# Kernel tuning notes

Measured on AMD Instinct MI355X. Metric: run time of the kernel, lower is better.

The kernel has to match this reference:

```python
import jax, jax.numpy as jnp
import numpy as np

N_NODES = 50000
N_EDGES = 600000
IN_DIM = 128
OUT_DIM = 128
EPS = 1e-12  # guards sqrt grad at exactly-zero diffs (matches torch.norm subgradient behavior)


def setup_inputs() -> dict:
    key = jax.random.key(0)
    k1, k2, k3, k4, k5 = jax.random.split(key, 5)
    h = jax.random.normal(k1, (N_NODES, IN_DIM), dtype=jnp.float32)
    # xavier-uniform-ish scale for fc weight [out_dim, in_dim]
    lim = float(np.sqrt(6.0 / (IN_DIM + OUT_DIM)))
    W_fc = jax.random.uniform(k2, (OUT_DIM, IN_DIM), dtype=jnp.float32, minval=-lim, maxval=lim)
    beta = jax.random.uniform(k3, (1,), dtype=jnp.float32)  # Tensor(1).uniform_(0,1)
    src = jax.random.randint(k4, (N_EDGES,), 0, N_NODES, dtype=jnp.int32)
    dst = jax.random.randint(k5, (N_EDGES,), 0, N_NODES, dtype=jnp.int32)
    return {"h": h, "W_fc": W_fc, "beta": beta, "src": src, "dst": dst}


def reference(h, W_fc, beta, src, dst):
    n = h.shape[0]
    # z = fc(h)  (dropout omitted for determinism; see notes)
    z = h @ W_fc.T  # [N, out_dim]
    zs = z[src]     # [E, out_dim] gather
    zd = z[dst]     # [E, out_dim] gather
    # RBF edge attention: e = -beta * ||z_src - z_dst||_2
    sq = jnp.sum((zs - zd) ** 2, axis=1)          # [E]
    e = -beta[0] * jnp.sqrt(sq + EPS)             # [E]
    # segment softmax over incoming edges of each dst node
    m = jax.ops.segment_max(e, dst, num_segments=n)   # [N], -inf for empty
    ex = jnp.exp(e - m[dst])                          # [E]
    denom = jax.ops.segment_sum(ex, dst, num_segments=n)  # [N]
    alpha = ex / denom[dst]                           # [E]
    # scatter-weighted sum of src features into dst nodes
    h_out = jax.ops.segment_sum(alpha[:, None] * zs, dst, num_segments=n)  # [N, out_dim]
    return h_out
```

## Files before the change

kernel.cpp:

```cpp
#include <hip/hip_runtime.h>
#include <math.h>

#define N_NODES 50000
#define N_EDGES 600000
#define DIM 128
#define BCAP 64

typedef __attribute__((ext_vector_type(8))) short bf16x8;
typedef __attribute__((ext_vector_type(4))) float f32x4;

static __device__ __forceinline__ short f2bf(float f) {
    unsigned u = __float_as_uint(f);
    unsigned r = (u + 0x7FFFu + ((u >> 16) & 1u)) >> 16;
    return (short)r;
}

#define UNPK(w, d0, d1)                         \
    d0 = __uint_as_float((w) << 16);            \
    d1 = __uint_as_float((w) & 0xFFFF0000u);

__global__ __launch_bounds__(256) void prep_kernel(const float* __restrict__ W,
                                                   unsigned short* __restrict__ Wb,
                                                   int* __restrict__ cur,
                                                   int* __restrict__ cnt) {
    int gid = blockIdx.x * 256 + threadIdx.x;
    if (gid < N_NODES) {
        cur[gid] = 0;
        cnt[gid] = 0;
    }
    if (gid < DIM * DIM) Wb[gid] = (unsigned short)f2bf(W[gid]);
}

__global__ __launch_bounds__(256) void bfill_kernel(const int* __restrict__ src,
                                                    const int* __restrict__ dst,
                                                    int* __restrict__ cur,
                                                    int* __restrict__ lst) {
    int i = blockIdx.x * 256 + threadIdx.x;
    if (i >= N_EDGES) return;
    int d = dst[i];
    int pos = atomicAdd(cur + d, 1);
    if (pos < BCAP) lst[d * BCAP + pos] = src[i];
}

__global__ __launch_bounds__(256) void count_kernel(const int* __restrict__ dst,
                                                    int* __restrict__ cnt) {
    int i = blockIdx.x * 256 + threadIdx.x;
    if (i < N_EDGES) atomicAdd(cnt + dst[i], 1);
}

__global__ __launch_bounds__(256) void scan_a(const int* __restrict__ cnt,
                                              int* __restrict__ incl,
                                              int* __restrict__ bsum) {
    __shared__ int s[256];
    int i = blockIdx.x * 256 + threadIdx.x;
    s[threadIdx.x] = (i < N_NODES) ? cnt[i] : 0;
    __syncthreads();
    #pragma unroll
    for (int off = 1; off < 256; off <<= 1) {
        int t = (threadIdx.x >= off) ? s[threadIdx.x - off] : 0;
        __syncthreads();
        s[threadIdx.x] += t;
        __syncthreads();
    }
    if (i < N_NODES) incl[i] = s[threadIdx.x];
    if (threadIdx.x == 255) bsum[blockIdx.x] = s[255];
}

__global__ __launch_bounds__(256) void scan_b(int* __restrict__ bsum, int nb) {
    __shared__ int s[256];
    s[threadIdx.x] = (threadIdx.x < nb) ? bsum[threadIdx.x] : 0;
    __syncthreads();
    #pragma unroll
    for (int off = 1; off < 256; off <<= 1) {
        int t = (threadIdx.x >= off) ? s[threadIdx.x - off] : 0;
        __syncthreads();
        s[threadIdx.x] += t;
        __syncthreads();
    }
    if (threadIdx.x < nb) bsum[threadIdx.x] = s[threadIdx.x];
}

__global__ __launch_bounds__(256) void scan_c(int* __restrict__ incl_off,
                                              const int* __restrict__ cnt,
                                              const int* __restrict__ bsum) {
    int i = blockIdx.x * 256 + threadIdx.x;
    if (i >= N_NODES) return;
    int base = (blockIdx.x > 0) ? bsum[blockIdx.x - 1] : 0;
    incl_off[i] = incl_off[i] - cnt[i] + base;
}

__global__ __launch_bounds__(256) void cfill_kernel(const int* __restrict__ src,
                                                    const int* __restrict__ dst,
                                                    const int* __restrict__ off,
                                                    int* __restrict__ cur,
                                                    int* __restrict__ lst) {
    int i = blockIdx.x * 256 + threadIdx.x;
    if (i >= N_EDGES) return;
    int d = dst[i];
    int pos = atomicAdd(cur + d, 1);
    lst[off[d] + pos] = src[i];
}

__global__ __launch_bounds__(256) void gemm_kernel(const float* __restrict__ h,
                                                   const unsigned short* __restrict__ Wb,
                                                   unsigned short* __restrict__ zb) {
    int wave = blockIdx.x * 4 + (threadIdx.x >> 6);
    if (wave >= N_NODES / 16) return;
    int lane = threadIdx.x & 63;
    int lo = lane & 15;
    int hi = lane >> 4;
    long row0 = (long)wave * 16;

    bf16x8 afrag[4];
    const float* arow = h + (row0 + lo) * DIM;
    #pragma unroll
    for (int kt = 0; kt < 4; ++kt) {
        const float* ap = arow + kt * 32 + hi * 8;
        float4 f0 = *(const float4*)ap;
        float4 f1 = *(const float4*)(ap + 4);
        bf16x8 a;
        a[0] = f2bf(f0.x); a[1] = f2bf(f0.y); a[2] = f2bf(f0.z); a[3] = f2bf(f0.w);
        a[4] = f2bf(f1.x); a[5] = f2bf(f1.y); a[6] = f2bf(f1.z); a[7] = f2bf(f1.w);
        afrag[kt] = a;
    }

    #pragma unroll
    for (int ct = 0; ct < 8; ++ct) {
        f32x4 acc = {0.f, 0.f, 0.f, 0.f};
        const unsigned short* brow = Wb + (ct * 16 + lo) * DIM + hi * 8;
        #pragma unroll
        for (int kt = 0; kt < 4; ++kt) {
            bf16x8 b = *(const bf16x8*)(brow + kt * 32);
            acc = __builtin_amdgcn_mfma_f32_16x16x32_bf16(afrag[kt], b, acc, 0, 0, 0);
        }
        unsigned short* zp = zb + (row0 + hi * 4) * DIM + ct * 16 + lo;
        zp[0 * DIM] = (unsigned short)f2bf(acc[0]);
        zp[1 * DIM] = (unsigned short)f2bf(acc[1]);
        zp[2 * DIM] = (unsigned short)f2bf(acc[2]);
        zp[3 * DIM] = (unsigned short)f2bf(acc[3]);
    }
}

__global__ __launch_bounds__(256) void node_kernel(const unsigned short* __restrict__ zb,
                                                   const int* __restrict__ lst,
                                                   const int* __restrict__ off,
                                                   const int* __restrict__ degp,
                                                   int stride,
                                                   const float* __restrict__ beta,
                                                   float* __restrict__ out) {
    int node = blockIdx.x * 4 + (threadIdx.x >> 6);
    if (node >= N_NODES) return;
    int lane = threadIdx.x & 63;
    int q = lane >> 4;
    int ql = lane & 15;
    int deg = degp[node];
    int start;
    if (stride > 0) {
        if (deg > BCAP) deg = BCAP;
        start = node * stride;
    } else {
        start = off[node];
    }
    float bet = beta[0];

    uint4 zdw = *(const uint4*)(zb + (long)node * DIM + ql * 8);
    float zd[8];
    UNPK(zdw.x, zd[0], zd[1]) UNPK(zdw.y, zd[2], zd[3])
    UNPK(zdw.z, zd[4], zd[5]) UNPK(zdw.w, zd[6], zd[7])

    float sden = 0.0f;
    float acc[8];
    #pragma unroll
    for (int i = 0; i < 8; ++i) acc[i] = 0.0f;

    for (int cb = 0; cb < deg; cb += 64) {
        int nch = deg - cb;
        if (nch > 64) nch = 64;
        int sj = (lane < nch) ? lst[start + cb + lane] : 0;

        for (int jb = 0; jb < nch; jb += 4) {
            int jo = jb + q;
            bool valid = jo < nch;
            int s = __shfl(sj, valid ? jo : 0, 64);
            uint4 aw = *(const uint4*)(zb + (long)s * DIM + ql * 8);
            float a[8];
            UNPK(aw.x, a[0], a[1]) UNPK(aw.y, a[2], a[3])
            UNPK(aw.z, a[4], a[5]) UNPK(aw.w, a[6], a[7])

            float p = 0.0f;
            #pragma unroll
            for (int i = 0; i < 8; ++i) {
                float d = a[i] - zd[i];
                p += d * d;
            }
            #pragma unroll
            for (int o = 1; o <= 8; o <<= 1) p += __shfl_xor(p, o, 64);
            float w = valid ? expf(-bet * sqrtf(p + 1e-12f)) : 0.0f;
            sden += w;
            #pragma unroll
            for (int i = 0; i < 8; ++i) acc[i] += w * a[i];
        }
    }

    #define CMB(v) v += __shfl_xor(v, 16, 64); v += __shfl_xor(v, 32, 64);
    CMB(sden)
    CMB(acc[0]) CMB(acc[1]) CMB(acc[2]) CMB(acc[3])
    CMB(acc[4]) CMB(acc[5]) CMB(acc[6]) CMB(acc[7])
    #undef CMB

    float inv = (deg > 0) ? 1.0f / sden : 0.0f;
    if (q == 0) {
        float* orow = out + (long)node * DIM + ql * 8;
        *(float4*)orow =
            make_float4(acc[0] * inv, acc[1] * inv, acc[2] * inv, acc[3] * inv);
        *(float4*)(orow + 4) =
            make_float4(acc[4] * inv, acc[5] * inv, acc[6] * inv, acc[7] * inv);
    }
}

extern "C" void kernel_launch(void* const* d_in, const int* in_sizes, int n_in,
                              void* d_out, int out_size, void* d_ws, size_t ws_size,
                              hipStream_t stream) {
    const float* h    = (const float*)d_in[0];
    const float* W    = (const float*)d_in[1];
    const float* beta = (const float*)d_in[2];
    const int* src    = (const int*)d_in[3];
    const int* dst    = (const int*)d_in[4];
    float* out = (float*)d_out;

    const size_t bucket_total = (3200000ull + 3200000 + 150000 + 256 + 8192) * 4;
    const bool use_bucket = ws_size >= bucket_total;
    const size_t lst_len = use_bucket ? 3200000 : 600000;

    float* ws  = (float*)d_ws;
    unsigned short* zb = (unsigned short*)ws;
    int* lst   = (int*)(ws + 3200000);
    int* cnt   = (int*)(ws + 3200000 + lst_len);
    int* cur   = cnt + 50000;
    int* off   = cur + 50000;
    int* bsum  = off + 50000;
    unsigned short* Wb = (unsigned short*)(bsum + 256);

    const int gemm_blocks = (N_NODES / 16 + 3) / 4;

    prep_kernel<<<196, 256, 0, stream>>>(W, Wb, cur, cnt);
    if (use_bucket) {
        bfill_kernel<<<(N_EDGES + 255) / 256, 256, 0, stream>>>(src, dst, cur, lst);
        gemm_kernel<<<gemm_blocks, 256, 0, stream>>>(h, Wb, zb);
        node_kernel<<<N_NODES / 4, 256, 0, stream>>>(zb, lst, cur , cur, BCAP,
                                                     beta, out);
    } else {
        count_kernel<<<(N_EDGES + 255) / 256, 256, 0, stream>>>(dst, cnt);
        scan_a<<<196, 256, 0, stream>>>(cnt, off, bsum);
        scan_b<<<1, 256, 0, stream>>>(bsum, 196);
        scan_c<<<196, 256, 0, stream>>>(off, cnt, bsum);
        cfill_kernel<<<(N_EDGES + 255) / 256, 256, 0, stream>>>(src, dst, off, cur, lst);
        gemm_kernel<<<gemm_blocks, 256, 0, stream>>>(h, Wb, zb);
        node_kernel<<<N_NODES / 4, 256, 0, stream>>>(zb, lst, off, cnt, 0, beta, out);
    }
}
```

Before: 167.7 us.

## Unroll neighbor gather by two and use DPP row reductions with fast math

The per-node aggregation loop now handles two groups of four neighbors per iteration, so two independent 16-byte gathers are in flight per lane. This is meant to hide memory latency. The 16-lane distance reduction uses DPP row-level adds instead of ds_swizzle/shfl_xor. The exact expf and sqrtf calls become __expf and the hardware sqrt intrinsic. The cost is more registers per thread and slightly lower precision in the attention weights.

```diff
diff --git a/kernel.cpp b/kernel.cpp
--- a/kernel.cpp
+++ b/kernel.cpp
@@ -18,6 +18,17 @@
 #define UNPK(w, d0, d1)                         \
     d0 = __uint_as_float((w) << 16);            \
     d1 = __uint_as_float((w) & 0xFFFF0000u);
+
+#define DPPADD(x, ctrl)                                                          \
+    x += __int_as_float(__builtin_amdgcn_mov_dpp(__float_as_int(x), ctrl,        \
+                                                 0xF, 0xF, true));
+static __device__ __forceinline__ float row_sum16(float x) {
+    DPPADD(x, 0xB1)
+    DPPADD(x, 0x4E)
+    DPPADD(x, 0x141)
+    DPPADD(x, 0x140)
+    return x;
+}
 
 __global__ __launch_bounds__(256) void prep_kernel(const float* __restrict__ W,
                                                    unsigned short* __restrict__ Wb,
@@ -161,7 +172,7 @@
     } else {
         start = off[node];
     }
-    float bet = beta[0];
+    float nbet = -beta[0];
 
     uint4 zdw = *(const uint4*)(zb + (long)node * DIM + ql * 8);
     float zd[8];
@@ -178,27 +189,36 @@
         if (nch > 64) nch = 64;
         int sj = (lane < nch) ? lst[start + cb + lane] : 0;
 
-        for (int jb = 0; jb < nch; jb += 4) {
-            int jo = jb + q;
-            bool valid = jo < nch;
-            int s = __shfl(sj, valid ? jo : 0, 64);
-            uint4 aw = *(const uint4*)(zb + (long)s * DIM + ql * 8);
-            float a[8];
-            UNPK(aw.x, a[0], a[1]) UNPK(aw.y, a[2], a[3])
-            UNPK(aw.z, a[4], a[5]) UNPK(aw.w, a[6], a[7])
-
-            float p = 0.0f;
+        for (int jb = 0; jb < nch; jb += 8) {
+            int jo0 = jb + q;
+            int jo1 = jb + 4 + q;
+            bool v0 = jo0 < nch;
+            bool v1 = jo1 < nch;
+            int s0 = __shfl(sj, v0 ? jo0 : 0, 64);
+            int s1 = __shfl(sj, v1 ? jo1 : 0, 64);
+            uint4 aw0 = *(const uint4*)(zb + (long)s0 * DIM + ql * 8);
+            uint4 aw1 = *(const uint4*)(zb + (long)s1 * DIM + ql * 8);
+            float a0[8], a1[8];
+            UNPK(aw0.x, a0[0], a0[1]) UNPK(aw0.y, a0[2], a0[3])
+            UNPK(aw0.z, a0[4], a0[5]) UNPK(aw0.w, a0[6], a0[7])
+            UNPK(aw1.x, a1[0], a1[1]) UNPK(aw1.y, a1[2], a1[3])
+            UNPK(aw1.z, a1[4], a1[5]) UNPK(aw1.w, a1[6], a1[7])
+
+            float p0 = 0.0f, p1 = 0.0f;
             #pragma unroll
             for (int i = 0; i < 8; ++i) {
-                float d = a[i] - zd[i];
-                p += d * d;
+                float d0 = a0[i] - zd[i];
+                p0 += d0 * d0;
+                float d1 = a1[i] - zd[i];
+                p1 += d1 * d1;
             }
+            p0 = row_sum16(p0);
+            p1 = row_sum16(p1);
+            float w0 = v0 ? __expf(nbet * __builtin_amdgcn_sqrtf(p0 + 1e-12f)) : 0.0f;
+            float w1 = v1 ? __expf(nbet * __builtin_amdgcn_sqrtf(p1 + 1e-12f)) : 0.0f;
+            sden += w0 + w1;
             #pragma unroll
-            for (int o = 1; o <= 8; o <<= 1) p += __shfl_xor(p, o, 64);
-            float w = valid ? expf(-bet * sqrtf(p + 1e-12f)) : 0.0f;
-            sden += w;
-            #pragma unroll
-            for (int i = 0; i < 8; ++i) acc[i] += w * a[i];
+            for (int i = 0; i < 8; ++i) acc[i] += w0 * a0[i] + w1 * a1[i];
         }
     }
 
```

After: 161.4 us. -3.8%, faster.

## Map one node per 16-lane group, DPP row reductions, packed transposed GEMM stores

Applied to the files above, without the earlier changes.

The node kernel now assigns each node to 16 lanes instead of a full 64-lane wave, so four nodes share a wave. This removes the cross-quarter combine shuffles and the idle lanes on low-degree nodes. The distance reduction uses DPP row operations instead of shfl_xor, and the kernel switches to fast exp, sqrt and rcp intrinsics. The GEMM swaps its MFMA operands so each lane writes a packed 8-byte store instead of four scattered 2-byte stores. In exchange, each node's edges are processed serially in its 16-lane group, which lowers memory-level parallelism per node and adds divergence across nodes of different degree.

```diff
diff --git a/kernel.cpp b/kernel.cpp
--- a/kernel.cpp
+++ b/kernel.cpp
@@ -18,6 +18,17 @@
 #define UNPK(w, d0, d1)                         \
     d0 = __uint_as_float((w) << 16);            \
     d1 = __uint_as_float((w) & 0xFFFF0000u);
+
+#define DPPADD(x, ctrl)                                                          \
+    x += __int_as_float(__builtin_amdgcn_mov_dpp(__float_as_int(x), ctrl,        \
+                                                 0xF, 0xF, true));
+static __device__ __forceinline__ float row_sum16(float x) {
+    DPPADD(x, 0xB1)
+    DPPADD(x, 0x4E)
+    DPPADD(x, 0x141)
+    DPPADD(x, 0x140)
+    return x;
+}
 
 __global__ __launch_bounds__(256) void prep_kernel(const float* __restrict__ W,
                                                    unsigned short* __restrict__ Wb,
@@ -109,35 +120,38 @@
     int lane = threadIdx.x & 63;
     int lo = lane & 15;
     int hi = lane >> 4;
-    long row0 = (long)wave * 16;
-
-    bf16x8 afrag[4];
-    const float* arow = h + (row0 + lo) * DIM;
+    long node0 = (long)wave * 16;
+
+    bf16x8 hfrag[4];
+    const float* hrow = h + (node0 + lo) * DIM;
     #pragma unroll
     for (int kt = 0; kt < 4; ++kt) {
-        const float* ap = arow + kt * 32 + hi * 8;
+        const float* ap = hrow + kt * 32 + hi * 8;
         float4 f0 = *(const float4*)ap;
         float4 f1 = *(const float4*)(ap + 4);
         bf16x8 a;
         a[0] = f2bf(f0.x); a[1] = f2bf(f0.y); a[2] = f2bf(f0.z); a[3] = f2bf(f0.w);
         a[4] = f2bf(f1.x); a[5] = f2bf(f1.y); a[6] = f2bf(f1.z); a[7] = f2bf(f1.w);
-        afrag[kt] = a;
-    }
-
-    #pragma unroll
-    for (int ct = 0; ct < 8; ++ct) {
+        hfrag[kt] = a;
+    }
+
+    #pragma unroll
+    for (int mt = 0; mt < 8; ++mt) {
         f32x4 acc = {0.f, 0.f, 0.f, 0.f};
-        const unsigned short* brow = Wb + (ct * 16 + lo) * DIM + hi * 8;
+        const unsigned short* wrow = Wb + (mt * 16 + lo) * DIM + hi * 8;
         #pragma unroll
         for (int kt = 0; kt < 4; ++kt) {
-            bf16x8 b = *(const bf16x8*)(brow + kt * 32);
-            acc = __builtin_amdgcn_mfma_f32_16x16x32_bf16(afrag[kt], b, acc, 0, 0, 0);
+            bf16x8 w = *(const bf16x8*)(wrow + kt * 32);
+            acc = __builtin_amdgcn_mfma_f32_16x16x32_bf16(w, hfrag[kt], acc, 0, 0, 0);
         }
-        unsigned short* zp = zb + (row0 + hi * 4) * DIM + ct * 16 + lo;
-        zp[0 * DIM] = (unsigned short)f2bf(acc[0]);
-        zp[1 * DIM] = (unsigned short)f2bf(acc[1]);
-        zp[2 * DIM] = (unsigned short)f2bf(acc[2]);
-        zp[3 * DIM] = (unsigned short)f2bf(acc[3]);
+        unsigned u0 = (unsigned)(unsigned short)f2bf(acc[0]);
+        unsigned u1 = (unsigned)(unsigned short)f2bf(acc[1]);
+        unsigned u2 = (unsigned)(unsigned short)f2bf(acc[2]);
+        unsigned u3 = (unsigned)(unsigned short)f2bf(acc[3]);
+        uint2 pk;
+        pk.x = u0 | (u1 << 16);
+        pk.y = u2 | (u3 << 16);
+        *(uint2*)(zb + (node0 + lo) * DIM + mt * 16 + hi * 4) = pk;
     }
 }
 
@@ -148,7 +162,7 @@
                                                    int stride,
                                                    const float* __restrict__ beta,
                                                    float* __restrict__ out) {
-    int node = blockIdx.x * 4 + (threadIdx.x >> 6);
+    int node = blockIdx.x * 16 + (threadIdx.x >> 4);
     if (node >= N_NODES) return;
     int lane = threadIdx.x & 63;
     int q = lane >> 4;
@@ -161,7 +175,7 @@
     } else {
         start = off[node];
     }
-    float bet = beta[0];
+    float nbet = -beta[0];
 
     uint4 zdw = *(const uint4*)(zb + (long)node * DIM + ql * 8);
     float zd[8];
@@ -173,15 +187,13 @@
     #pragma unroll
     for (int i = 0; i < 8; ++i) acc[i] = 0.0f;
 
-    for (int cb = 0; cb < deg; cb += 64) {
+    for (int cb = 0; cb < deg; cb += 16) {
         int nch = deg - cb;
-        if (nch > 64) nch = 64;
-        int sj = (lane < nch) ? lst[start + cb + lane] : 0;
-
-        for (int jb = 0; jb < nch; jb += 4) {
-            int jo = jb + q;
-            bool valid = jo < nch;
-            int s = __shfl(sj, valid ? jo : 0, 64);
+        if (nch > 16) nch = 16;
+        int sj = (ql < nch) ? lst[start + cb + ql] : 0;
+
+        for (int j = 0; j < nch; ++j) {
+            int s = __shfl(sj, (q << 4) | j, 64);
             uint4 aw = *(const uint4*)(zb + (long)s * DIM + ql * 8);
             float a[8];
             UNPK(aw.x, a[0], a[1]) UNPK(aw.y, a[2], a[3])
@@ -193,29 +205,20 @@
                 float d = a[i] - zd[i];
                 p += d * d;
             }
-            #pragma unroll
-            for (int o = 1; o <= 8; o <<= 1) p += __shfl_xor(p, o, 64);
-            float w = valid ? expf(-bet * sqrtf(p + 1e-12f)) : 0.0f;
+            p = row_sum16(p);
+            float w = __expf(nbet * __builtin_amdgcn_sqrtf(p + 1e-12f));
             sden += w;
             #pragma unroll
             for (int i = 0; i < 8; ++i) acc[i] += w * a[i];
         }
     }
 
-    #define CMB(v) v += __shfl_xor(v, 16, 64); v += __shfl_xor(v, 32, 64);
-    CMB(sden)
-    CMB(acc[0]) CMB(acc[1]) CMB(acc[2]) CMB(acc[3])
-    CMB(acc[4]) CMB(acc[5]) CMB(acc[6]) CMB(acc[7])
-    #undef CMB
-
-    float inv = (deg > 0) ? 1.0f / sden : 0.0f;
-    if (q == 0) {
-        float* orow = out + (long)node * DIM + ql * 8;
-        *(float4*)orow =
-            make_float4(acc[0] * inv, acc[1] * inv, acc[2] * inv, acc[3] * inv);
-        *(float4*)(orow + 4) =
-            make_float4(acc[4] * inv, acc[5] * inv, acc[6] * inv, acc[7] * inv);
-    }
+    float inv = (deg > 0) ? __builtin_amdgcn_rcpf(sden) : 0.0f;
+    float* orow = out + (long)node * DIM + ql * 8;
+    *(float4*)orow =
+        make_float4(acc[0] * inv, acc[1] * inv, acc[2] * inv, acc[3] * inv);
+    *(float4*)(orow + 4) =
+        make_float4(acc[4] * inv, acc[5] * inv, acc[6] * inv, acc[7] * inv);
 }
 
 extern "C" void kernel_launch(void* const* d_in, const int* in_sizes, int n_in,
@@ -242,12 +245,13 @@
     unsigned short* Wb = (unsigned short*)(bsum + 256);
 
     const int gemm_blocks = (N_NODES / 16 + 3) / 4;
+    const int node_blocks = (N_NODES + 15) / 16;
 
     prep_kernel<<<196, 256, 0, stream>>>(W, Wb, cur, cnt);
     if (use_bucket) {
         bfill_kernel<<<(N_EDGES + 255) / 256, 256, 0, stream>>>(src, dst, cur, lst);
         gemm_kernel<<<gemm_blocks, 256, 0, stream>>>(h, Wb, zb);
-        node_kernel<<<N_NODES / 4, 256, 0, stream>>>(zb, lst, cur , cur, BCAP,
+        node_kernel<<<node_blocks, 256, 0, stream>>>(zb, lst, cur , cur, BCAP,
                                                      beta, out);
     } else {
         count_kernel<<<(N_EDGES + 255) / 256, 256, 0, stream>>>(dst, cnt);
@@ -256,6 +260,6 @@
         scan_c<<<196, 256, 0, stream>>>(off, cnt, bsum);
         cfill_kernel<<<(N_EDGES + 255) / 256, 256, 0, stream>>>(src, dst, off, cur, lst);
         gemm_kernel<<<gemm_blocks, 256, 0, stream>>>(h, Wb, zb);
-        node_kernel<<<N_NODES / 4, 256, 0, stream>>>(zb, lst, off, cnt, 0, beta, out);
-    }
-}
+        node_kernel<<<node_blocks, 256, 0, stream>>>(zb, lst, off, cnt, 0, beta, out);
+    }
+}
```

Result: faster. 164.1 us (-2.2%).
